# Performance work log

Measured on AMD Instinct MI355X. Metric: run time of the kernel, lower is better.

## Reference

```python
import jax, jax.numpy as jnp
import numpy as np

BATCH, SEQ_LEN, D_MODEL, STATE_N, N_CLASSES = 32, 4096, 256, 64, 5


def setup_inputs() -> dict:
    key = jax.random.key(0)
    ks = jax.random.split(key, 9)
    x = jax.random.normal(ks[0], (BATCH, SEQ_LEN), jnp.float32)
    w_in = jax.random.normal(ks[1], (D_MODEL,), jnp.float32)
    b_in = jax.random.normal(ks[2], (D_MODEL,), jnp.float32) * 0.1
    # stable diagonal transition in (0.9, 0.999)
    A_diag = 0.9 + 0.099 * jax.random.uniform(ks[3], (D_MODEL, STATE_N), jnp.float32)
    B_in = jax.random.normal(ks[4], (D_MODEL, STATE_N), jnp.float32) * 0.1
    C_out = jax.random.normal(ks[5], (D_MODEL, STATE_N), jnp.float32) * 0.1
    D_skip = jax.random.normal(ks[6], (D_MODEL,), jnp.float32)
    W_head = jax.random.normal(ks[7], (2 * D_MODEL, N_CLASSES), jnp.float32) * 0.05
    b_head = jnp.zeros((N_CLASSES,), jnp.float32)
    return {"x": x, "w_in": w_in, "b_in": b_in, "A_diag": A_diag, "B_in": B_in,
            "C_out": C_out, "D_skip": D_skip, "W_head": W_head, "b_head": b_head}


def reference(x, w_in, b_in, A_diag, B_in, C_out, D_skip, W_head, b_head):
    # x: [B, T] scalar ECG signal; diagonal SSM recurrence over T via lax.scan
    Bsz = x.shape[0]
    D, N = A_diag.shape

    def step(s, xt):
        # xt: [B] scalar input at time t; project to channels
        u = xt[:, None] * w_in + b_in              # [B, D]
        s = A_diag * s + B_in * u[:, :, None]      # [B, D, N]
        h = jax.nn.gelu(jnp.einsum('bdn,dn->bd', s, C_out) + D_skip * u)  # [B, D]
        return s, h

    s0 = jnp.zeros((Bsz, D, N), x.dtype)
    _, h_all = jax.lax.scan(step, s0, x.T)         # h_all: [T, B, D]
    avg_p = h_all.mean(axis=0)                     # [B, D]
    max_p = h_all.max(axis=0)                      # [B, D]
    pooled = jnp.concatenate([avg_p, max_p], axis=-1)  # [B, 2D] (streaming_pool='avgmax')
    return pooled @ W_head + b_head                # [B, n_classes]
```

## Files before the change

### kernel.cpp

```cpp
#include <hip/hip_runtime.h>

#define BATCH 32
#define SEQ 4096
#define DMODEL 256
#define NCLS 5

typedef short          s8v  __attribute__((ext_vector_type(8)));
typedef unsigned short u8v  __attribute__((ext_vector_type(8)));
typedef unsigned short u4v  __attribute__((ext_vector_type(4)));
typedef float          f4v  __attribute__((ext_vector_type(4)));

__device__ __forceinline__ unsigned short f2b(float f) {
    unsigned u = __float_as_uint(f);
    u += 0x7FFFu + ((u >> 16) & 1u);
    return (unsigned short)(u >> 16);
}
__device__ __forceinline__ float dpp_shr4(float v) {
    return __int_as_float(__builtin_amdgcn_update_dpp(
        0, __float_as_int(v), 0x114, 0xF, 0xF, true));
}
__device__ __forceinline__ float dpp_shr8(float v) {
    return __int_as_float(__builtin_amdgcn_update_dpp(
        0, __float_as_int(v), 0x118, 0xF, 0xF, true));
}
__device__ __forceinline__ float swz_or12(float v) {
    return __int_as_float(__builtin_amdgcn_ds_swizzle(
        __float_as_int(v), 0x019F));
}

__global__ __launch_bounds__(512) void ssm_mfma_kernel(
    const float* __restrict__ x,
    const float* __restrict__ w_in,
    const float* __restrict__ b_in,
    const float* __restrict__ A_diag,
    const float* __restrict__ B_in,
    const float* __restrict__ C_out,
    const float* __restrict__ D_skip,
    float* __restrict__ pooled)
{
    __shared__ float          Pow [65 * 64];
    __shared__ unsigned short MAb [64 * 72];
    __shared__ unsigned short CATb[64 * 72];
    __shared__ unsigned short TGb [64 * 72];
    __shared__ unsigned short Xb  [128 * 72];
    __shared__ unsigned short Sigb[128 * 72];
    __shared__ float Pf[64], Qf[64], Gf[64], Hf[64], HcpS[64], Anf[64];

    const int tid  = threadIdx.x;
    const int lane = tid & 63;
    const int wid  = tid >> 6;
    const int m16  = lane & 15;
    const int q    = lane >> 4;
    const int q4   = q * 4;
    const int q8   = q * 8;
    const int d    = blockIdx.x;

    const float wd = w_in[d], bd = b_in[d];
    const float Dw = D_skip[d] * wd;
    const float Db = D_skip[d] * bd;

    const int bcol = wid * 4 + (m16 & 3);
    const int cch  = m16 >> 2;
    const int pcol = wid * 16 + m16;
    const float* xrow = x + bcol * SEQ + cch * 64 + q * 16;
    unsigned short* xdst = &Xb[pcol * 72 + q * 16];

    float4 xl0 = ((const float4*)xrow)[0];
    float4 xl1 = ((const float4*)xrow)[1];
    float4 xl2 = ((const float4*)xrow)[2];
    float4 xl3 = ((const float4*)xrow)[3];

    if (tid < 64) {
        const int n = tid;
        const float An = A_diag[d * 64 + n];
        const float CB = B_in[d * 64 + n] * C_out[d * 64 + n];
        Anf[n] = An; Pf[n] = CB * wd; Qf[n] = CB * bd;
        float p = 1.0f;
        for (int m = 0; m <= 64; ++m) { Pow[m * 64 + n] = p; p *= An; }
    }
    __syncthreads();
    {
        const int mrow = tid >> 3, p8 = (tid & 7) * 8;
        float g = 0.0f, h = 0.0f;
        #pragma unroll
        for (int jj = 0; jj < 8; ++jj) {
            const float pw = Pow[mrow * 64 + p8 + jj];
            g = fmaf(pw, Pf[p8 + jj], g);
            h = fmaf(pw, Qf[p8 + jj], h);
        }
        g += __shfl_xor(g, 1, 64); g += __shfl_xor(g, 2, 64); g += __shfl_xor(g, 4, 64);
        h += __shfl_xor(h, 1, 64); h += __shfl_xor(h, 2, 64); h += __shfl_xor(h, 4, 64);
        if ((tid & 7) == 0) { Gf[mrow] = g; Hf[mrow] = h; }
    }
    __syncthreads();
    {
        const int r0 = tid >> 3, c0 = (tid & 7) * 8;
        #pragma unroll
        for (int jj = 0; jj < 8; ++jj) {
            const int j = c0 + jj;
            MAb [r0 * 72 + j] = f2b(Pf[r0] * Pow[(63 - j) * 64 + r0]);
            CATb[r0 * 72 + j] = f2b(Pow[(r0 + 1) * 64 + j]);
            TGb [r0 * 72 + j] = (j < r0)  ? f2b(Gf[r0 - j])
                              : (j == r0) ? f2b(Gf[0] + Dw)
                                          : (unsigned short)0;
        }
        if (tid < 64) {
            float v = Hf[tid];
            #pragma unroll
            for (int dl = 1; dl < 64; dl <<= 1) {
                const float t = __shfl(v, (tid - dl) & 63, 64);
                v += (tid >= dl) ? t : 0.0f;
            }
            HcpS[tid] = v + Db;
        }
    }
    __syncthreads();

    s8v aMA[4][2], aCAT[4][2], aTG[4][2];
    #pragma unroll
    for (int rt = 0; rt < 4; ++rt)
        #pragma unroll
        for (int kb = 0; kb < 2; ++kb) {
            const int off = (rt * 16 + m16) * 72 + kb * 32 + q8;
            aMA [rt][kb] = *(const s8v*)&MAb [off];
            aCAT[rt][kb] = *(const s8v*)&CATb[off];
            aTG [rt][kb] = *(const s8v*)&TGb [off];
        }
    f4v cq[4], hcp[4];
    float a64v[4][4], sig0[4][4];
    #pragma unroll
    for (int rt = 0; rt < 4; ++rt)
        #pragma unroll
        for (int r = 0; r < 4; ++r) {
            const int nn = rt * 16 + q4 + r;
            const float A64 = Pow[64 * 64 + nn];
            a64v[rt][r] = A64;
            cq[rt][r]   = Qf[nn] * (1.0f - A64) / (1.0f - Anf[nn]);
            hcp[rt][r]  = HcpS[nn];
            sig0[rt][r] = 0.0f;
        }
    const bool cc1 = (cch & 1) != 0;
    const bool cc2 = (cch & 2) != 0;

    {
        u8v lo, hi;
        lo[0]=f2b(xl0.x); lo[1]=f2b(xl0.y); lo[2]=f2b(xl0.z); lo[3]=f2b(xl0.w);
        lo[4]=f2b(xl1.x); lo[5]=f2b(xl1.y); lo[6]=f2b(xl1.z); lo[7]=f2b(xl1.w);
        hi[0]=f2b(xl2.x); hi[1]=f2b(xl2.y); hi[2]=f2b(xl2.z); hi[3]=f2b(xl2.w);
        hi[4]=f2b(xl3.x); hi[5]=f2b(xl3.y); hi[6]=f2b(xl3.z); hi[7]=f2b(xl3.w);
        *(u8v*)xdst       = lo;
        *(u8v*)(xdst + 8) = hi;
    }

    float psum = 0.0f, pmax = -1e30f;

    #pragma unroll 1
    for (int g = 0; g < 16; ++g) {
        float4 yl0, yl1, yl2, yl3;
        if (g < 15) {
            const float4* xg = (const float4*)(xrow + (g + 1) * 256);
            yl0 = xg[0]; yl1 = xg[1]; yl2 = xg[2]; yl3 = xg[3];
        }
        const s8v bx0 = *(const s8v*)&Xb[pcol * 72 + q8];
        const s8v bx1 = *(const s8v*)&Xb[pcol * 72 + 32 + q8];
        f4v vB[4];
        #pragma unroll
        for (int rt = 0; rt < 4; ++rt) {
            vB[rt] = __builtin_amdgcn_mfma_f32_16x16x32_bf16(aMA[rt][0], bx0, cq[rt], 0, 0, 0);
            vB[rt] = __builtin_amdgcn_mfma_f32_16x16x32_bf16(aMA[rt][1], bx1, vB[rt], 0, 0, 0);
        }
        if (g < 15) {
            u8v lo, hi;
            lo[0]=f2b(yl0.x); lo[1]=f2b(yl0.y); lo[2]=f2b(yl0.z); lo[3]=f2b(yl0.w);
            lo[4]=f2b(yl1.x); lo[5]=f2b(yl1.y); lo[6]=f2b(yl1.z); lo[7]=f2b(yl1.w);
            hi[0]=f2b(yl2.x); hi[1]=f2b(yl2.y); hi[2]=f2b(yl2.z); hi[3]=f2b(yl2.w);
            hi[4]=f2b(yl3.x); hi[5]=f2b(yl3.y); hi[6]=f2b(yl3.z); hi[7]=f2b(yl3.w);
            *(u8v*)xdst       = lo;
            *(u8v*)(xdst + 8) = hi;
        }
        #pragma unroll
        for (int rt = 0; rt < 4; ++rt) {
            u4v sg;
            #pragma unroll
            for (int r = 0; r < 4; ++r) {
                const float a  = a64v[rt][r];
                const float a2 = a * a;
                const float v  = vB[rt][r];
                const float t1 = dpp_shr4(v);
                const float i1 = fmaf(a, t1, v);
                const float t2 = dpp_shr8(i1);
                const float e  = fmaf(a, t2, t1);
                const float ac = (cc1 ? a : 1.0f) * (cc2 ? a2 : 1.0f);
                const float se = fmaf(ac, sig0[rt][r], e);
                const float i2 = fmaf(a, e, v);
                const float S  = swz_or12(i2);
                sig0[rt][r] = fmaf(a2 * a2, sig0[rt][r], S);
                sg[r] = f2b(se);
            }
            *(u4v*)&Sigb[pcol * 72 + rt * 16 + q4] = sg;
        }
        const s8v bs0 = *(const s8v*)&Sigb[pcol * 72 + q8];
        const s8v bs1 = *(const s8v*)&Sigb[pcol * 72 + 32 + q8];
        #pragma unroll
        for (int rt = 0; rt < 4; ++rt) {
            f4v acc = __builtin_amdgcn_mfma_f32_16x16x32_bf16(aCAT[rt][0], bs0, hcp[rt], 0, 0, 0);
            acc = __builtin_amdgcn_mfma_f32_16x16x32_bf16(aCAT[rt][1], bs1, acc, 0, 0, 0);
            acc = __builtin_amdgcn_mfma_f32_16x16x32_bf16(aTG [rt][0], bx0, acc, 0, 0, 0);
            acc = __builtin_amdgcn_mfma_f32_16x16x32_bf16(aTG [rt][1], bx1, acc, 0, 0, 0);
            #pragma unroll
            for (int r = 0; r < 4; ++r) {
                const float yt = acc[r];
                const float y2 = yt * yt;
                const float zn = yt * fmaf(-0.07135481627f, y2, -1.5957691216f);
                const float h  = yt * __builtin_amdgcn_rcpf(1.0f + __expf(zn));
                psum += h;
                pmax = fmaxf(pmax, h);
            }
        }
    }

    #pragma unroll
    for (int dl = 4; dl <= 32; dl <<= 1) {
        psum += __shfl_xor(psum, dl, 64);
        pmax  = fmaxf(pmax, __shfl_xor(pmax, dl, 64));
    }
    if (lane < 4) {
        const int b = wid * 4 + lane;
        pooled[b * (2 * DMODEL) + d]          = psum * (1.0f / SEQ);
        pooled[b * (2 * DMODEL) + DMODEL + d] = pmax;
    }
}

__global__ __launch_bounds__(64) void head_kernel(
    const float* __restrict__ pooled,
    const float* __restrict__ W_head,
    const float* __restrict__ b_head,
    float* __restrict__ out)
{
    const int b = blockIdx.x, l = threadIdx.x;
    const float* p = pooled + b * (2 * DMODEL);
    float acc[NCLS] = {0, 0, 0, 0, 0};
    for (int k = l; k < 2 * DMODEL; k += 64) {
        const float pv = p[k];
        #pragma unroll
        for (int c = 0; c < NCLS; ++c)
            acc[c] = fmaf(pv, W_head[k * NCLS + c], acc[c]);
    }
    #pragma unroll
    for (int off = 32; off; off >>= 1)
        #pragma unroll
        for (int c = 0; c < NCLS; ++c) acc[c] += __shfl_xor(acc[c], off, 64);
    if (l == 0)
        #pragma unroll
        for (int c = 0; c < NCLS; ++c) out[b * NCLS + c] = acc[c] + b_head[c];
}

extern "C" void kernel_launch(void* const* d_in, const int* in_sizes, int n_in,
                              void* d_out, int out_size, void* d_ws, size_t ws_size,
                              hipStream_t stream) {
    const float* x      = (const float*)d_in[0];
    const float* w_in   = (const float*)d_in[1];
    const float* b_in   = (const float*)d_in[2];
    const float* A_diag = (const float*)d_in[3];
    const float* B_in   = (const float*)d_in[4];
    const float* C_out  = (const float*)d_in[5];
    const float* D_skip = (const float*)d_in[6];
    const float* W_head = (const float*)d_in[7];
    const float* b_head = (const float*)d_in[8];
    float* pooled = (float*)d_ws;
    float* out    = (float*)d_out;

    ssm_mfma_kernel<<<DMODEL, 512, 0, stream>>>(x, w_in, b_in, A_diag, B_in,
                                                C_out, D_skip, pooled);
    head_kernel<<<BATCH, 64, 0, stream>>>(pooled, W_head, b_head, out);
}
```

Before: 108.9 us.

## Split batch across two blocks per channel, share work across wave pairs, fuse head via atomics

```diff
diff --git a/kernel.cpp b/kernel.cpp
--- a/kernel.cpp
+++ b/kernel.cpp
@@ -1,4 +1,5 @@
 #include <hip/hip_runtime.h>
+#include <hip/hip_bf16.h>
 
 #define BATCH 32
 #define SEQ 4096
@@ -6,14 +7,12 @@
 #define NCLS 5
 
 typedef short          s8v  __attribute__((ext_vector_type(8)));
-typedef unsigned short u8v  __attribute__((ext_vector_type(8)));
 typedef unsigned short u4v  __attribute__((ext_vector_type(4)));
 typedef float          f4v  __attribute__((ext_vector_type(4)));
 
-__device__ __forceinline__ unsigned short f2b(float f) {
-    unsigned u = __float_as_uint(f);
-    u += 0x7FFFu + ((u >> 16) & 1u);
-    return (unsigned short)(u >> 16);
+__device__ __forceinline__ unsigned short f2bs(float f) {
+    __hip_bfloat16 h = __float2bfloat16(f);
+    return *reinterpret_cast<unsigned short*>(&h);
 }
 __device__ __forceinline__ float dpp_shr4(float v) {
     return __int_as_float(__builtin_amdgcn_update_dpp(
@@ -28,7 +27,7 @@
         __float_as_int(v), 0x019F));
 }
 
-__global__ __launch_bounds__(512) void ssm_mfma_kernel(
+__global__ __launch_bounds__(512, 4) void ssm_mfma_kernel(
     const float* __restrict__ x,
     const float* __restrict__ w_in,
     const float* __restrict__ b_in,
@@ -36,15 +35,18 @@
     const float* __restrict__ B_in,
     const float* __restrict__ C_out,
     const float* __restrict__ D_skip,
-    float* __restrict__ pooled)
+    const float* __restrict__ W_head,
+    const float* __restrict__ b_head,
+    float* __restrict__ out)
 {
     __shared__ float          Pow [65 * 64];
     __shared__ unsigned short MAb [64 * 72];
     __shared__ unsigned short CATb[64 * 72];
     __shared__ unsigned short TGb [64 * 72];
-    __shared__ unsigned short Xb  [128 * 72];
-    __shared__ unsigned short Sigb[128 * 72];
-    __shared__ float Pf[64], Qf[64], Gf[64], Hf[64], HcpS[64], Anf[64];
+    __shared__ unsigned short Xb  [64 * 72];
+    __shared__ unsigned short Sigb[64 * 72];
+    __shared__ float Pf[64], Qf[64], Gf[64], Hf[64], HcpS[64], Anf[64], cqS[64];
+    __shared__ float psA[16], pmA[16], psB[16], pmB[16];
 
     const int tid  = threadIdx.x;
     const int lane = tid & 63;
@@ -53,22 +55,28 @@
     const int q    = lane >> 4;
     const int q4   = q * 4;
     const int q8   = q * 8;
-    const int d    = blockIdx.x;
+    const int d    = blockIdx.x >> 1;
+    const int bh   = blockIdx.x & 1;
+
+    const int pair = wid >> 1;
+    const int nh   = wid & 1;
+    const int nb   = nh * 32;
+    const int tb   = nh * 32;
+    const int pcol = pair * 16 + m16;
 
     const float wd = w_in[d], bd = b_in[d];
     const float Dw = D_skip[d] * wd;
     const float Db = D_skip[d] * bd;
 
-    const int bcol = wid * 4 + (m16 & 3);
-    const int cch  = m16 >> 2;
-    const int pcol = wid * 16 + m16;
-    const float* xrow = x + bcol * SEQ + cch * 64 + q * 16;
-    unsigned short* xdst = &Xb[pcol * 72 + q * 16];
+    const int cg    = tid >> 3;
+    const int j0    = (tid & 7) * 8;
+    const int bglob = bh * 16 + (cg >> 4) * 4 + (cg & 3);
+    const int cch   = (cg & 15) >> 2;
+    const float* xrow = x + bglob * SEQ + cch * 64 + j0;
+    unsigned short* xdst = &Xb[cg * 72 + j0];
 
     float4 xl0 = ((const float4*)xrow)[0];
     float4 xl1 = ((const float4*)xrow)[1];
-    float4 xl2 = ((const float4*)xrow)[2];
-    float4 xl3 = ((const float4*)xrow)[3];
 
     if (tid < 64) {
         const int n = tid;
@@ -98,10 +106,10 @@
         #pragma unroll
         for (int jj = 0; jj < 8; ++jj) {
             const int j = c0 + jj;
-            MAb [r0 * 72 + j] = f2b(Pf[r0] * Pow[(63 - j) * 64 + r0]);
-            CATb[r0 * 72 + j] = f2b(Pow[(r0 + 1) * 64 + j]);
-            TGb [r0 * 72 + j] = (j < r0)  ? f2b(Gf[r0 - j])
-                              : (j == r0) ? f2b(Gf[0] + Dw)
+            MAb [r0 * 72 + j] = f2bs(Pf[r0] * Pow[(63 - j) * 64 + r0]);
+            CATb[r0 * 72 + j] = f2bs(Pow[(r0 + 1) * 64 + j]);
+            TGb [r0 * 72 + j] = (j < r0)  ? f2bs(Gf[r0 - j])
+                              : (j == r0) ? f2bs(Gf[0] + Dw)
                                           : (unsigned short)0;
         }
         if (tid < 64) {
@@ -112,98 +120,99 @@
                 v += (tid >= dl) ? t : 0.0f;
             }
             HcpS[tid] = v + Db;
-        }
-    }
-    __syncthreads();
-
-    s8v aMA[4][2], aCAT[4][2], aTG[4][2];
+            const float A64 = Pow[64 * 64 + tid];
+            cqS[tid] = Qf[tid] * (1.0f - A64) / (1.0f - Anf[tid]);
+        }
+    }
+    __syncthreads();
+
+    s8v aMA[2][2], aCAT[2][2], aTG[2][2];
     #pragma unroll
-    for (int rt = 0; rt < 4; ++rt)
+    for (int rt = 0; rt < 2; ++rt)
         #pragma unroll
         for (int kb = 0; kb < 2; ++kb) {
-            const int off = (rt * 16 + m16) * 72 + kb * 32 + q8;
-            aMA [rt][kb] = *(const s8v*)&MAb [off];
-            aCAT[rt][kb] = *(const s8v*)&CATb[off];
-            aTG [rt][kb] = *(const s8v*)&TGb [off];
-        }
-    f4v cq[4], hcp[4];
-    float a64v[4][4], sig0[4][4];
+            aMA [rt][kb] = *(const s8v*)&MAb [(nb + rt * 16 + m16) * 72 + kb * 32 + q8];
+            aCAT[rt][kb] = *(const s8v*)&CATb[(tb + rt * 16 + m16) * 72 + kb * 32 + q8];
+            aTG [rt][kb] = *(const s8v*)&TGb [(tb + rt * 16 + m16) * 72 + kb * 32 + q8];
+        }
+    float a64v[2][4], acv[2][4], sig0[2][4];
+    const int cc = m16 >> 2;
     #pragma unroll
-    for (int rt = 0; rt < 4; ++rt)
+    for (int rt = 0; rt < 2; ++rt)
         #pragma unroll
         for (int r = 0; r < 4; ++r) {
-            const int nn = rt * 16 + q4 + r;
-            const float A64 = Pow[64 * 64 + nn];
-            a64v[rt][r] = A64;
-            cq[rt][r]   = Qf[nn] * (1.0f - A64) / (1.0f - Anf[nn]);
-            hcp[rt][r]  = HcpS[nn];
+            const int nn = nb + rt * 16 + q4 + r;
+            const float a = Pow[64 * 64 + nn];
+            a64v[rt][r] = a;
+            const float a2 = a * a;
+            acv [rt][r] = ((cc & 1) ? a : 1.0f) * ((cc & 2) ? a2 : 1.0f);
             sig0[rt][r] = 0.0f;
         }
-    const bool cc1 = (cch & 1) != 0;
-    const bool cc2 = (cch & 2) != 0;
 
     {
-        u8v lo, hi;
-        lo[0]=f2b(xl0.x); lo[1]=f2b(xl0.y); lo[2]=f2b(xl0.z); lo[3]=f2b(xl0.w);
-        lo[4]=f2b(xl1.x); lo[5]=f2b(xl1.y); lo[6]=f2b(xl1.z); lo[7]=f2b(xl1.w);
-        hi[0]=f2b(xl2.x); hi[1]=f2b(xl2.y); hi[2]=f2b(xl2.z); hi[3]=f2b(xl2.w);
-        hi[4]=f2b(xl3.x); hi[5]=f2b(xl3.y); hi[6]=f2b(xl3.z); hi[7]=f2b(xl3.w);
-        *(u8v*)xdst       = lo;
-        *(u8v*)(xdst + 8) = hi;
-    }
+        uint4 w;
+        w.x = (unsigned)f2bs(xl0.x) | ((unsigned)f2bs(xl0.y) << 16);
+        w.y = (unsigned)f2bs(xl0.z) | ((unsigned)f2bs(xl0.w) << 16);
+        w.z = (unsigned)f2bs(xl1.x) | ((unsigned)f2bs(xl1.y) << 16);
+        w.w = (unsigned)f2bs(xl1.z) | ((unsigned)f2bs(xl1.w) << 16);
+        *(uint4*)xdst = w;
+    }
+    __syncthreads();
 
     float psum = 0.0f, pmax = -1e30f;
 
     #pragma unroll 1
     for (int g = 0; g < 16; ++g) {
-        float4 yl0, yl1, yl2, yl3;
+        float4 yl0, yl1;
         if (g < 15) {
             const float4* xg = (const float4*)(xrow + (g + 1) * 256);
-            yl0 = xg[0]; yl1 = xg[1]; yl2 = xg[2]; yl3 = xg[3];
+            yl0 = xg[0]; yl1 = xg[1];
         }
         const s8v bx0 = *(const s8v*)&Xb[pcol * 72 + q8];
         const s8v bx1 = *(const s8v*)&Xb[pcol * 72 + 32 + q8];
-        f4v vB[4];
-        #pragma unroll
-        for (int rt = 0; rt < 4; ++rt) {
-            vB[rt] = __builtin_amdgcn_mfma_f32_16x16x32_bf16(aMA[rt][0], bx0, cq[rt], 0, 0, 0);
+        f4v vB[2];
+        #pragma unroll
+        for (int rt = 0; rt < 2; ++rt) {
+            const f4v cqv = *(const f4v*)&cqS[nb + rt * 16 + q4];
+            vB[rt] = __builtin_amdgcn_mfma_f32_16x16x32_bf16(aMA[rt][0], bx0, cqv, 0, 0, 0);
             vB[rt] = __builtin_amdgcn_mfma_f32_16x16x32_bf16(aMA[rt][1], bx1, vB[rt], 0, 0, 0);
         }
-        if (g < 15) {
-            u8v lo, hi;
-            lo[0]=f2b(yl0.x); lo[1]=f2b(yl0.y); lo[2]=f2b(yl0.z); lo[3]=f2b(yl0.w);
-            lo[4]=f2b(yl1.x); lo[5]=f2b(yl1.y); lo[6]=f2b(yl1.z); lo[7]=f2b(yl1.w);
-            hi[0]=f2b(yl2.x); hi[1]=f2b(yl2.y); hi[2]=f2b(yl2.z); hi[3]=f2b(yl2.w);
-            hi[4]=f2b(yl3.x); hi[5]=f2b(yl3.y); hi[6]=f2b(yl3.z); hi[7]=f2b(yl3.w);
-            *(u8v*)xdst       = lo;
-            *(u8v*)(xdst + 8) = hi;
-        }
-        #pragma unroll
-        for (int rt = 0; rt < 4; ++rt) {
+        #pragma unroll
+        for (int rt = 0; rt < 2; ++rt) {
             u4v sg;
             #pragma unroll
             for (int r = 0; r < 4; ++r) {
                 const float a  = a64v[rt][r];
-                const float a2 = a * a;
                 const float v  = vB[rt][r];
                 const float t1 = dpp_shr4(v);
                 const float i1 = fmaf(a, t1, v);
                 const float t2 = dpp_shr8(i1);
                 const float e  = fmaf(a, t2, t1);
-                const float ac = (cc1 ? a : 1.0f) * (cc2 ? a2 : 1.0f);
-                const float se = fmaf(ac, sig0[rt][r], e);
+                const float se = fmaf(acv[rt][r], sig0[rt][r], e);
                 const float i2 = fmaf(a, e, v);
                 const float S  = swz_or12(i2);
+                const float a2 = a * a;
                 sig0[rt][r] = fmaf(a2 * a2, sig0[rt][r], S);
-                sg[r] = f2b(se);
+                sg[r] = f2bs(se);
             }
-            *(u4v*)&Sigb[pcol * 72 + rt * 16 + q4] = sg;
-        }
+            *(u4v*)&Sigb[pcol * 72 + nb + rt * 16 + q4] = sg;
+        }
+        __syncthreads();
+
         const s8v bs0 = *(const s8v*)&Sigb[pcol * 72 + q8];
         const s8v bs1 = *(const s8v*)&Sigb[pcol * 72 + 32 + q8];
-        #pragma unroll
-        for (int rt = 0; rt < 4; ++rt) {
-            f4v acc = __builtin_amdgcn_mfma_f32_16x16x32_bf16(aCAT[rt][0], bs0, hcp[rt], 0, 0, 0);
+        if (g < 15) {
+            uint4 w;
+            w.x = (unsigned)f2bs(yl0.x) | ((unsigned)f2bs(yl0.y) << 16);
+            w.y = (unsigned)f2bs(yl0.z) | ((unsigned)f2bs(yl0.w) << 16);
+            w.z = (unsigned)f2bs(yl1.x) | ((unsigned)f2bs(yl1.y) << 16);
+            w.w = (unsigned)f2bs(yl1.z) | ((unsigned)f2bs(yl1.w) << 16);
+            *(uint4*)xdst = w;
+        }
+        #pragma unroll
+        for (int rt = 0; rt < 2; ++rt) {
+            const f4v hcpv = *(const f4v*)&HcpS[tb + rt * 16 + q4];
+            f4v acc = __builtin_amdgcn_mfma_f32_16x16x32_bf16(aCAT[rt][0], bs0, hcpv, 0, 0, 0);
             acc = __builtin_amdgcn_mfma_f32_16x16x32_bf16(aCAT[rt][1], bs1, acc, 0, 0, 0);
             acc = __builtin_amdgcn_mfma_f32_16x16x32_bf16(aTG [rt][0], bx0, acc, 0, 0, 0);
             acc = __builtin_amdgcn_mfma_f32_16x16x32_bf16(aTG [rt][1], bx1, acc, 0, 0, 0);
@@ -217,6 +226,7 @@
                 pmax = fmaxf(pmax, h);
             }
         }
+        __syncthreads();
     }
 
     #pragma unroll
@@ -225,34 +235,23 @@
         pmax  = fmaxf(pmax, __shfl_xor(pmax, dl, 64));
     }
     if (lane < 4) {
-        const int b = wid * 4 + lane;
-        pooled[b * (2 * DMODEL) + d]          = psum * (1.0f / SEQ);
-        pooled[b * (2 * DMODEL) + DMODEL + d] = pmax;
-    }
-}
-
-__global__ __launch_bounds__(64) void head_kernel(
-    const float* __restrict__ pooled,
-    const float* __restrict__ W_head,
-    const float* __restrict__ b_head,
-    float* __restrict__ out)
-{
-    const int b = blockIdx.x, l = threadIdx.x;
-    const float* p = pooled + b * (2 * DMODEL);
-    float acc[NCLS] = {0, 0, 0, 0, 0};
-    for (int k = l; k < 2 * DMODEL; k += 64) {
-        const float pv = p[k];
-        #pragma unroll
-        for (int c = 0; c < NCLS; ++c)
-            acc[c] = fmaf(pv, W_head[k * NCLS + c], acc[c]);
-    }
-    #pragma unroll
-    for (int off = 32; off; off >>= 1)
-        #pragma unroll
-        for (int c = 0; c < NCLS; ++c) acc[c] += __shfl_xor(acc[c], off, 64);
-    if (l == 0)
-        #pragma unroll
-        for (int c = 0; c < NCLS; ++c) out[b * NCLS + c] = acc[c] + b_head[c];
+        const int idx = pair * 4 + lane;
+        if (nh == 0) { psA[idx] = psum; pmA[idx] = pmax; }
+        else         { psB[idx] = psum; pmB[idx] = pmax; }
+    }
+    __syncthreads();
+    if (tid < 16) {
+        const int bg = bh * 16 + tid;
+        const float s  = (psA[tid] + psB[tid]) * (1.0f / SEQ);
+        const float mx = fmaxf(pmA[tid], pmB[tid]);
+        #pragma unroll
+        for (int c = 0; c < NCLS; ++c) {
+            float contrib = s  * W_head[d * NCLS + c]
+                          + mx * W_head[(DMODEL + d) * NCLS + c];
+            if (d == 0) contrib += b_head[c];
+            atomicAdd(&out[bg * NCLS + c], contrib);
+        }
+    }
 }
 
 extern "C" void kernel_launch(void* const* d_in, const int* in_sizes, int n_in,
@@ -267,10 +266,9 @@
     const float* D_skip = (const float*)d_in[6];
     const float* W_head = (const float*)d_in[7];
     const float* b_head = (const float*)d_in[8];
-    float* pooled = (float*)d_ws;
-    float* out    = (float*)d_out;
-
-    ssm_mfma_kernel<<<DMODEL, 512, 0, stream>>>(x, w_in, b_in, A_diag, B_in,
-                                                C_out, D_skip, pooled);
-    head_kernel<<<BATCH, 64, 0, stream>>>(pooled, W_head, b_head, out);
-}
+    float* out = (float*)d_out;
+
+    hipMemsetAsync(out, 0, BATCH * NCLS * sizeof(float), stream);
+    ssm_mfma_kernel<<<DMODEL * 2, 512, 0, stream>>>(x, w_in, b_in, A_diag, B_in,
+                                                    C_out, D_skip, W_head, b_head, out);
+}
```

Result: slower. 132.7 us (+21.8%).

## Fuse classifier head into SSM kernel via atomics and alias shared buffers

Applied to the files above, without the earlier changes.

```diff
diff --git a/kernel.cpp b/kernel.cpp
--- a/kernel.cpp
+++ b/kernel.cpp
@@ -1,4 +1,5 @@
 #include <hip/hip_runtime.h>
+#include <hip/hip_bf16.h>
 
 #define BATCH 32
 #define SEQ 4096
@@ -10,10 +11,9 @@
 typedef unsigned short u4v  __attribute__((ext_vector_type(4)));
 typedef float          f4v  __attribute__((ext_vector_type(4)));
 
-__device__ __forceinline__ unsigned short f2b(float f) {
-    unsigned u = __float_as_uint(f);
-    u += 0x7FFFu + ((u >> 16) & 1u);
-    return (unsigned short)(u >> 16);
+__device__ __forceinline__ unsigned short f2bs(float f) {
+    __hip_bfloat16 h = __float2bfloat16(f);
+    return *reinterpret_cast<unsigned short*>(&h);
 }
 __device__ __forceinline__ float dpp_shr4(float v) {
     return __int_as_float(__builtin_amdgcn_update_dpp(
@@ -36,15 +36,19 @@
     const float* __restrict__ B_in,
     const float* __restrict__ C_out,
     const float* __restrict__ D_skip,
-    float* __restrict__ pooled)
+    const float* __restrict__ W_head,
+    const float* __restrict__ b_head,
+    float* __restrict__ out)
 {
-    __shared__ float          Pow [65 * 64];
+    __shared__ __align__(16) unsigned char XSbuf[2 * 128 * 72 * 2];
     __shared__ unsigned short MAb [64 * 72];
     __shared__ unsigned short CATb[64 * 72];
     __shared__ unsigned short TGb [64 * 72];
-    __shared__ unsigned short Xb  [128 * 72];
-    __shared__ unsigned short Sigb[128 * 72];
     __shared__ float Pf[64], Qf[64], Gf[64], Hf[64], HcpS[64], Anf[64];
+
+    unsigned short* Xb   = (unsigned short*)XSbuf;
+    unsigned short* Sigb = (unsigned short*)(XSbuf + 128 * 72 * 2);
+    float*          Pow  = (float*)XSbuf;
 
     const int tid  = threadIdx.x;
     const int lane = tid & 63;
@@ -98,10 +102,10 @@
         #pragma unroll
         for (int jj = 0; jj < 8; ++jj) {
             const int j = c0 + jj;
-            MAb [r0 * 72 + j] = f2b(Pf[r0] * Pow[(63 - j) * 64 + r0]);
-            CATb[r0 * 72 + j] = f2b(Pow[(r0 + 1) * 64 + j]);
-            TGb [r0 * 72 + j] = (j < r0)  ? f2b(Gf[r0 - j])
-                              : (j == r0) ? f2b(Gf[0] + Dw)
+            MAb [r0 * 72 + j] = f2bs(Pf[r0] * Pow[(63 - j) * 64 + r0]);
+            CATb[r0 * 72 + j] = f2bs(Pow[(r0 + 1) * 64 + j]);
+            TGb [r0 * 72 + j] = (j < r0)  ? f2bs(Gf[r0 - j])
+                              : (j == r0) ? f2bs(Gf[0] + Dw)
                                           : (unsigned short)0;
         }
         if (tid < 64) {
@@ -141,14 +145,15 @@
         }
     const bool cc1 = (cch & 1) != 0;
     const bool cc2 = (cch & 2) != 0;
+    __syncthreads();
 
     {
         u8v lo, hi;
-        lo[0]=f2b(xl0.x); lo[1]=f2b(xl0.y); lo[2]=f2b(xl0.z); lo[3]=f2b(xl0.w);
-        lo[4]=f2b(xl1.x); lo[5]=f2b(xl1.y); lo[6]=f2b(xl1.z); lo[7]=f2b(xl1.w);
-        hi[0]=f2b(xl2.x); hi[1]=f2b(xl2.y); hi[2]=f2b(xl2.z); hi[3]=f2b(xl2.w);
-        hi[4]=f2b(xl3.x); hi[5]=f2b(xl3.y); hi[6]=f2b(xl3.z); hi[7]=f2b(xl3.w);
-        *(u8v*)xdst       = lo;
+        lo[0]=f2bs(xl0.x); lo[1]=f2bs(xl0.y); lo[2]=f2bs(xl0.z); lo[3]=f2bs(xl0.w);
+        lo[4]=f2bs(xl1.x); lo[5]=f2bs(xl1.y); lo[6]=f2bs(xl1.z); lo[7]=f2bs(xl1.w);
+        hi[0]=f2bs(xl2.x); hi[1]=f2bs(xl2.y); hi[2]=f2bs(xl2.z); hi[3]=f2bs(xl2.w);
+        hi[4]=f2bs(xl3.x); hi[5]=f2bs(xl3.y); hi[6]=f2bs(xl3.z); hi[7]=f2bs(xl3.w);
+        *(u8v*)(xdst)     = lo;
         *(u8v*)(xdst + 8) = hi;
     }
 
@@ -171,11 +176,11 @@
         }
         if (g < 15) {
             u8v lo, hi;
-            lo[0]=f2b(yl0.x); lo[1]=f2b(yl0.y); lo[2]=f2b(yl0.z); lo[3]=f2b(yl0.w);
-            lo[4]=f2b(yl1.x); lo[5]=f2b(yl1.y); lo[6]=f2b(yl1.z); lo[7]=f2b(yl1.w);
-            hi[0]=f2b(yl2.x); hi[1]=f2b(yl2.y); hi[2]=f2b(yl2.z); hi[3]=f2b(yl2.w);
-            hi[4]=f2b(yl3.x); hi[5]=f2b(yl3.y); hi[6]=f2b(yl3.z); hi[7]=f2b(yl3.w);
-            *(u8v*)xdst       = lo;
+            lo[0]=f2bs(yl0.x); lo[1]=f2bs(yl0.y); lo[2]=f2bs(yl0.z); lo[3]=f2bs(yl0.w);
+            lo[4]=f2bs(yl1.x); lo[5]=f2bs(yl1.y); lo[6]=f2bs(yl1.z); lo[7]=f2bs(yl1.w);
+            hi[0]=f2bs(yl2.x); hi[1]=f2bs(yl2.y); hi[2]=f2bs(yl2.z); hi[3]=f2bs(yl2.w);
+            hi[4]=f2bs(yl3.x); hi[5]=f2bs(yl3.y); hi[6]=f2bs(yl3.z); hi[7]=f2bs(yl3.w);
+            *(u8v*)(xdst)     = lo;
             *(u8v*)(xdst + 8) = hi;
         }
         #pragma unroll
@@ -184,18 +189,18 @@
             #pragma unroll
             for (int r = 0; r < 4; ++r) {
                 const float a  = a64v[rt][r];
-                const float a2 = a * a;
                 const float v  = vB[rt][r];
                 const float t1 = dpp_shr4(v);
                 const float i1 = fmaf(a, t1, v);
                 const float t2 = dpp_shr8(i1);
                 const float e  = fmaf(a, t2, t1);
-                const float ac = (cc1 ? a : 1.0f) * (cc2 ? a2 : 1.0f);
+                const float ac = (cc1 ? a : 1.0f) * (cc2 ? a * a : 1.0f);
                 const float se = fmaf(ac, sig0[rt][r], e);
                 const float i2 = fmaf(a, e, v);
                 const float S  = swz_or12(i2);
+                const float a2 = a * a;
                 sig0[rt][r] = fmaf(a2 * a2, sig0[rt][r], S);
-                sg[r] = f2b(se);
+                sg[r] = f2bs(se);
             }
             *(u4v*)&Sigb[pcol * 72 + rt * 16 + q4] = sg;
         }
@@ -211,8 +216,8 @@
             for (int r = 0; r < 4; ++r) {
                 const float yt = acc[r];
                 const float y2 = yt * yt;
-                const float zn = yt * fmaf(-0.07135481627f, y2, -1.5957691216f);
-                const float h  = yt * __builtin_amdgcn_rcpf(1.0f + __expf(zn));
+                const float zn = yt * fmaf(-0.10294272f, y2, -2.30220437f);
+                const float h  = yt * __builtin_amdgcn_rcpf(1.0f + exp2f(zn));
                 psum += h;
                 pmax = fmaxf(pmax, h);
             }
@@ -226,33 +231,15 @@
     }
     if (lane < 4) {
         const int b = wid * 4 + lane;
-        pooled[b * (2 * DMODEL) + d]          = psum * (1.0f / SEQ);
-        pooled[b * (2 * DMODEL) + DMODEL + d] = pmax;
-    }
-}
-
-__global__ __launch_bounds__(64) void head_kernel(
-    const float* __restrict__ pooled,
-    const float* __restrict__ W_head,
-    const float* __restrict__ b_head,
-    float* __restrict__ out)
-{
-    const int b = blockIdx.x, l = threadIdx.x;
-    const float* p = pooled + b * (2 * DMODEL);
-    float acc[NCLS] = {0, 0, 0, 0, 0};
-    for (int k = l; k < 2 * DMODEL; k += 64) {
-        const float pv = p[k];
-        #pragma unroll
-        for (int c = 0; c < NCLS; ++c)
-            acc[c] = fmaf(pv, W_head[k * NCLS + c], acc[c]);
-    }
-    #pragma unroll
-    for (int off = 32; off; off >>= 1)
-        #pragma unroll
-        for (int c = 0; c < NCLS; ++c) acc[c] += __shfl_xor(acc[c], off, 64);
-    if (l == 0)
-        #pragma unroll
-        for (int c = 0; c < NCLS; ++c) out[b * NCLS + c] = acc[c] + b_head[c];
+        const float s = psum * (1.0f / SEQ);
+        #pragma unroll
+        for (int c = 0; c < NCLS; ++c) {
+            float contrib = s    * W_head[d * NCLS + c]
+                          + pmax * W_head[(DMODEL + d) * NCLS + c];
+            if (d == 0) contrib += b_head[c];
+            atomicAdd(&out[b * NCLS + c], contrib);
+        }
+    }
 }
 
 extern "C" void kernel_launch(void* const* d_in, const int* in_sizes, int n_in,
@@ -267,10 +254,9 @@
     const float* D_skip = (const float*)d_in[6];
     const float* W_head = (const float*)d_in[7];
     const float* b_head = (const float*)d_in[8];
-    float* pooled = (float*)d_ws;
-    float* out    = (float*)d_out;
-
+    float* out = (float*)d_out;
+
+    hipMemsetAsync(out, 0, BATCH * NCLS * sizeof(float), stream);
     ssm_mfma_kernel<<<DMODEL, 512, 0, stream>>>(x, w_in, b_in, A_diag, B_in,
-                                                C_out, D_skip, pooled);
-    head_kernel<<<BATCH, 64, 0, stream>>>(pooled, W_head, b_head, out);
-}
+                                                C_out, D_skip, W_head, b_head, out);
+}
```

After: 168.6 us. 54.8% more time.
